# Kernel tuning notes

Measured on AMD Instinct MI355X. Metric: run time of the kernel, lower is better.

The kernel has to match this reference:

```python
import jax, jax.numpy as jnp
import numpy as np

EMBED_DIM = 768
NUM_HEADS = 12
HEAD_DIM = EMBED_DIM // NUM_HEADS
SCALE = HEAD_DIM ** -0.5


def setup_inputs() -> dict:
    key = jax.random.key(0)
    k_x, k_qw, k_qb, k_pw, k_pb = jax.random.split(key, 5)
    B, N, C = 8, 1024, EMBED_DIM
    std = C ** -0.5
    return {
        "x": jax.random.normal(k_x, (B, N, C), dtype=jnp.float32),
        "qkv_w": jax.random.normal(k_qw, (C, 3 * C), dtype=jnp.float32) * std,
        "qkv_b": jax.random.normal(k_qb, (3 * C,), dtype=jnp.float32) * 0.02,
        "proj_w": jax.random.normal(k_pw, (C, C), dtype=jnp.float32) * std,
        "proj_b": jax.random.normal(k_pb, (C,), dtype=jnp.float32) * 0.02,
    }


def reference(x, qkv_w, qkv_b, proj_w, proj_b):
    B, N, C = x.shape
    # QKV projection: [B,N,3C] -> [3,B,H,N,Dh]
    qkv = (x @ qkv_w + qkv_b).reshape(B, N, 3, NUM_HEADS, HEAD_DIM)
    qkv = jnp.transpose(qkv, (2, 0, 3, 1, 4))
    q, k, v = qkv[0], qkv[1], qkv[2]
    # attention scores [B,H,N,N]
    attn = jnp.einsum("bhqd,bhkd->bhqk", q, k) * SCALE
    attn_weights = jax.nn.softmax(attn, axis=-1)
    # dropout=0.0 (eval) -> identity
    out = jnp.einsum("bhqk,bhkd->bhqd", attn_weights, v)
    out = jnp.transpose(out, (0, 2, 1, 3)).reshape(B, N, C)
    out = out @ proj_w + proj_b
    return out, attn_weights
```

## Files before the change

### kernel.cpp

```cpp
#include <hip/hip_runtime.h>
#include <cstdint>
#include <cstddef>

namespace {

constexpr int B = 8, NSEQ = 1024, C = 768, H = 12, D = 64, N3 = 2304;
constexpr float SCALE = 0.125f;
constexpr size_t QKV_ELEMS = (size_t)B * H * NSEQ * D;

using f32x4 = __attribute__((ext_vector_type(4))) float;
using s16x8 = __attribute__((ext_vector_type(8))) short;

__device__ __forceinline__ unsigned short f2bf(float f) {
  union { float f; uint32_t u; } v; v.f = f;
  const uint32_t r = v.u + 0x7FFFu + ((v.u >> 16) & 1u);
  return (unsigned short)(r >> 16);
}
__device__ __forceinline__ float bf2f(unsigned short s) {
  union { uint32_t u; float f; } v; v.u = ((uint32_t)s) << 16;
  return v.f;
}
__device__ __forceinline__ void gload_lds16(const void* g, void* l) {
  __builtin_amdgcn_global_load_lds(
      (const __attribute__((address_space(1))) uint32_t*)g,
      (__attribute__((address_space(3))) uint32_t*)l, 16, 0, 0);
}

__global__ void cvt_x(const float* __restrict__ x, unsigned short* __restrict__ xb, int n4) {
  const int stride = gridDim.x * 256;
  for (int idx = blockIdx.x * 256 + threadIdx.x; idx < n4; idx += stride) {
    const float4 v = ((const float4*)x)[idx];
    ushort4 o;
    o.x = f2bf(v.x); o.y = f2bf(v.y); o.z = f2bf(v.z); o.w = f2bf(v.w);
    ((ushort4*)xb)[idx] = o;
  }
}

__global__ void transp_cvt(const float* __restrict__ w, unsigned short* __restrict__ wt,
                           int K, int N) {
  __shared__ float t[32][33];
  const int n0 = blockIdx.x << 5, k0 = blockIdx.y << 5;
  const int tid = threadIdx.x;
  #pragma unroll
  for (int r = 0; r < 4; ++r) {
    const int e = (r << 8) + tid;
    const int kk = e >> 5, nn = e & 31;
    t[kk][nn] = w[(size_t)(k0 + kk) * N + n0 + nn];
  }
  __syncthreads();
  #pragma unroll
  for (int r = 0; r < 4; ++r) {
    const int e = (r << 8) + tid;
    const int nn = e >> 5, kk = e & 31;
    wt[(size_t)(n0 + nn) * K + k0 + kk] = f2bf(t[kk][nn]);
  }
}

template<int MODE>
__global__ __launch_bounds__(256, 2)
void gemm_bf16(const unsigned short* __restrict__ A,
               const unsigned short* __restrict__ Wt,
               const float* __restrict__ bias,
               unsigned short* __restrict__ qp, unsigned short* __restrict__ kp,
               unsigned short* __restrict__ vt, float* __restrict__ out32,
               int M, int N) {
  constexpr int K = 768;
  __shared__ short As[128 * 64];
  __shared__ short Bs[128 * 64];
  const int tid = threadIdx.x;
  const int wid = tid >> 6, lane = tid & 63;
  const int wm = wid >> 1, wn = wid & 1;
  const int lg = lane >> 4, lr = lane & 15;
  const int m0 = blockIdx.y << 7, n0 = blockIdx.x << 7;

  f32x4 acc[4][4] = {};

  for (int k0 = 0; k0 < K; k0 += 64) {
    __syncthreads();
    #pragma unroll
    for (int r = 0; r < 4; ++r) {
      const int c = (r << 8) + tid;
      const int row = c >> 3, g8 = c & 7;
      const int gp = g8 ^ (row & 7);
      const int ldsoff = (((r << 8) + (wid << 6)) << 3);
      gload_lds16(A + (size_t)(m0 + row) * K + k0 + (gp << 3), (void*)(As + ldsoff));
      gload_lds16(Wt + (size_t)(n0 + row) * K + k0 + (gp << 3), (void*)(Bs + ldsoff));
    }
    __syncthreads();
    #pragma unroll
    for (int kc = 0; kc < 2; ++kc) {
      s16x8 af[4], bf[4];
      #pragma unroll
      for (int i = 0; i < 4; ++i) {
        const int ra = (wm << 6) + (i << 4) + lr;
        const int ca = ((kc << 2) + lg) ^ (ra & 7);
        af[i] = *(const s16x8*)(As + (ra << 6) + (ca << 3));
        const int rb = (wn << 6) + (i << 4) + lr;
        const int cb = ((kc << 2) + lg) ^ (rb & 7);
        bf[i] = *(const s16x8*)(Bs + (rb << 6) + (cb << 3));
      }
      #pragma unroll
      for (int i = 0; i < 4; ++i)
        #pragma unroll
        for (int j = 0; j < 4; ++j)
          acc[i][j] = __builtin_amdgcn_mfma_f32_16x16x32_bf16(af[i], bf[j], acc[i][j], 0, 0, 0);
    }
  }

  #pragma unroll
  for (int i = 0; i < 4; ++i) {
    const int m = m0 + (wm << 6) + (i << 4) + (lg << 2);
    #pragma unroll
    for (int j = 0; j < 4; ++j) {
      const int n = n0 + (wn << 6) + (j << 4) + lr;
      const float bv = bias[n];
      if (MODE == 0) {
        const int which = (n >= 1536) ? 2 : (n >= 768 ? 1 : 0);
        const int hh = (n - which * 768) >> 6;
        const int d = n & 63;
        const int b = m >> 10, ns = m & 1023;
        const size_t bh = (size_t)b * H + hh;
        if (which < 2) {
          unsigned short* dst = (which == 0 ? qp : kp) + (bh * NSEQ + ns) * D + d;
          #pragma unroll
          for (int rg = 0; rg < 4; ++rg)
            dst[(size_t)rg * D] = f2bf(acc[i][j][rg] + bv);
        } else {
          ushort4 pk;
          pk.x = f2bf(acc[i][j][0] + bv);
          pk.y = f2bf(acc[i][j][1] + bv);
          pk.z = f2bf(acc[i][j][2] + bv);
          pk.w = f2bf(acc[i][j][3] + bv);
          *(ushort4*)(vt + (bh * D + d) * NSEQ + ns) = pk;
        }
      } else {
        float* dst = out32 + (size_t)m * N + n;
        #pragma unroll
        for (int rg = 0; rg < 4; ++rg)
          dst[(size_t)rg * N] = acc[i][j][rg] + bv;
      }
    }
  }
}

__global__ __launch_bounds__(256, 3)
void attn_mfma(const unsigned short* __restrict__ qg,
               const unsigned short* __restrict__ kg,
               const unsigned short* __restrict__ vtg,
               float* __restrict__ attnw,
               unsigned short* __restrict__ aout) {
  __shared__ short sc[16][1032];
  __shared__ short kv[64 * 64];
  __shared__ float invs[16];
  const int tid = threadIdx.x;
  const int wid = tid >> 6, lane = tid & 63;
  const int lg = lane >> 4, lr = lane & 15;
  const int bh = blockIdx.y;
  const int q0 = blockIdx.x << 4;
  const size_t kvbase = (size_t)bh * NSEQ * D;

  s16x8 qf[2];
  #pragma unroll
  for (int kc = 0; kc < 2; ++kc)
    qf[kc] = *(const s16x8*)(qg + kvbase + (size_t)(q0 + lr) * D + (kc << 5) + (lg << 3));

  for (int j0 = 0; j0 < NSEQ; j0 += 64) {
    __syncthreads();
    #pragma unroll
    for (int r = 0; r < 2; ++r) {
      const int c = (r << 8) + tid;
      const int row = c >> 3, g8 = c & 7;
      gload_lds16(kg + kvbase + (size_t)(j0 + row) * D + ((g8 ^ (row & 7)) << 3),
                  (void*)(kv + (((r << 8) + (wid << 6)) << 3)));
    }
    __syncthreads();
    f32x4 cacc = {};
    const int krow = (wid << 4) + lr;
    #pragma unroll
    for (int kc = 0; kc < 2; ++kc) {
      const int cg = ((kc << 2) + lg) ^ (krow & 7);
      const s16x8 kf = *(const s16x8*)(kv + (krow << 6) + (cg << 3));
      cacc = __builtin_amdgcn_mfma_f32_16x16x32_bf16(qf[kc], kf, cacc, 0, 0, 0);
    }
    const int jglob = j0 + (wid << 4) + lr;
    #pragma unroll
    for (int rg = 0; rg < 4; ++rg)
      sc[(lg << 2) + rg][jglob] = (short)f2bf(cacc[rg] * SCALE);
  }
  __syncthreads();

  {
    const int row = tid >> 4, ql = tid & 15;
    float mx = -3.0e38f;
    #pragma unroll
    for (int c = 0; c < 8; ++c) {
      const s16x8 v = *(const s16x8*)(&sc[row][(ql << 3) + (c << 7)]);
      #pragma unroll
      for (int e = 0; e < 8; ++e) mx = fmaxf(mx, bf2f((unsigned short)v[e]));
    }
    #pragma unroll
    for (int off = 8; off > 0; off >>= 1) mx = fmaxf(mx, __shfl_xor(mx, off, 16));
    float s = 0.f;
    #pragma unroll
    for (int c = 0; c < 8; ++c) {
      s16x8 v = *(s16x8*)(&sc[row][(ql << 3) + (c << 7)]);
      #pragma unroll
      for (int e = 0; e < 8; ++e) {
        const float ev = __expf(bf2f((unsigned short)v[e]) - mx);
        s += ev;
        v[e] = (short)f2bf(ev);
      }
      *(s16x8*)(&sc[row][(ql << 3) + (c << 7)]) = v;
    }
    #pragma unroll
    for (int off = 8; off > 0; off >>= 1) s += __shfl_xor(s, off, 16);
    if (ql == 0) invs[row] = 1.0f / s;
  }
  __syncthreads();

  {
    float* wbase = attnw + ((size_t)bh * NSEQ + q0) * NSEQ;
    #pragma unroll
    for (int r = 0; r < 16; ++r) {
      const float iv = invs[r];
      const ushort4 e4 = *(const ushort4*)(&sc[r][tid << 2]);
      float4 o;
      o.x = bf2f(e4.x) * iv; o.y = bf2f(e4.y) * iv;
      o.z = bf2f(e4.z) * iv; o.w = bf2f(e4.w) * iv;
      *(float4*)(wbase + (size_t)r * NSEQ + (tid << 2)) = o;
    }
  }

  f32x4 oacc = {};
  for (int j0 = 0; j0 < NSEQ; j0 += 64) {
    __syncthreads();
    #pragma unroll
    for (int r = 0; r < 2; ++r) {
      const int c = (r << 8) + tid;
      const int row = c >> 3, g8 = c & 7;
      gload_lds16(vtg + (size_t)bh * D * NSEQ + (size_t)row * NSEQ + j0 + ((g8 ^ (row & 7)) << 3),
                  (void*)(kv + (((r << 8) + (wid << 6)) << 3)));
    }
    __syncthreads();
    const int drow = (wid << 4) + lr;
    #pragma unroll
    for (int kc = 0; kc < 2; ++kc) {
      const s16x8 pa = *(const s16x8*)(&sc[lr][j0 + (kc << 5) + (lg << 3)]);
      const int cg = ((kc << 2) + lg) ^ (drow & 7);
      const s16x8 vf = *(const s16x8*)(kv + (drow << 6) + (cg << 3));
      oacc = __builtin_amdgcn_mfma_f32_16x16x32_bf16(pa, vf, oacc, 0, 0, 0);
    }
  }
  {
    const int b = bh / H, hh = bh - b * H;
    const int d = (wid << 4) + lr;
    #pragma unroll
    for (int rg = 0; rg < 4; ++rg) {
      const int i = (lg << 2) + rg;
      aout[((size_t)b * NSEQ + q0 + i) * C + hh * D + d] = f2bf(oacc[rg] * invs[i]);
    }
  }
}

}

extern "C" void kernel_launch(void* const* d_in, const int* in_sizes, int n_in,
                              void* d_out, int out_size, void* d_ws, size_t ws_size,
                              hipStream_t stream) {
  const float* x      = (const float*)d_in[0];
  const float* qkv_w  = (const float*)d_in[1];
  const float* qkv_b  = (const float*)d_in[2];
  const float* proj_w = (const float*)d_in[3];
  const float* proj_b = (const float*)d_in[4];

  float* out   = (float*)d_out;
  float* attnw = out + (size_t)B * NSEQ * C;

  unsigned short* xb   = (unsigned short*)d_ws;
  unsigned short* wtq  = xb   + (size_t)8192 * 768;
  unsigned short* wtp  = wtq  + (size_t)2304 * 768;
  unsigned short* qp   = wtp  + (size_t)768 * 768;
  unsigned short* kp   = qp   + QKV_ELEMS;
  unsigned short* vtp  = kp   + QKV_ELEMS;
  unsigned short* wsao = vtp  + QKV_ELEMS;

  cvt_x<<<1024, 256, 0, stream>>>(x, xb, (int)((size_t)8192 * 768 / 4));
  transp_cvt<<<dim3(N3 / 32, C / 32), 256, 0, stream>>>(qkv_w, wtq, C, N3);
  transp_cvt<<<dim3(C / 32, C / 32), 256, 0, stream>>>(proj_w, wtp, C, C);

  gemm_bf16<0><<<dim3(N3 / 128, 8192 / 128), 256, 0, stream>>>(
      xb, wtq, qkv_b, qp, kp, vtp, nullptr, 8192, N3);

  attn_mfma<<<dim3(NSEQ / 16, B * H), 256, 0, stream>>>(qp, kp, vtp, attnw, wsao);

  gemm_bf16<1><<<dim3(C / 128, 8192 / 128), 256, 0, stream>>>(
      wsao, wtp, proj_b, nullptr, nullptr, nullptr, out, 8192, C);
}
```

Baseline: 266.6 us.

## Double attention query tile per block and remap blocks across XCDs

The attention kernel now runs 512 threads and handles 32 query rows per block. Each K/V tile loaded into shared memory therefore serves two 16-row query groups, which halves K/V reloads per query. Block indices in both the attention and GEMM kernels are remapped so that neighbouring logical tiles land on the same XCD, aiming for better L2 reuse of shared operands. The attention-weight store moves after the PV product and is widened to 8 elements per thread. The cost is a larger shared-memory footprint (32 score rows) and lower occupancy per block.

After: 283.8 us. 6.4% more time.

```diff
diff --git a/kernel.cpp b/kernel.cpp
--- a/kernel.cpp
+++ b/kernel.cpp
@@ -26,7 +26,8 @@
       (__attribute__((address_space(3))) uint32_t*)l, 16, 0, 0);
 }
 
-__global__ void cvt_x(const float* __restrict__ x, unsigned short* __restrict__ xb, int n4) {
+__global__ __launch_bounds__(256)
+void cvt_x(const float* __restrict__ x, unsigned short* __restrict__ xb, int n4) {
   const int stride = gridDim.x * 256;
   for (int idx = blockIdx.x * 256 + threadIdx.x; idx < n4; idx += stride) {
     const float4 v = ((const float4*)x)[idx];
@@ -36,8 +37,9 @@
   }
 }
 
-__global__ void transp_cvt(const float* __restrict__ w, unsigned short* __restrict__ wt,
-                           int K, int N) {
+__global__ __launch_bounds__(256)
+void transp_cvt(const float* __restrict__ w, unsigned short* __restrict__ wt,
+                int K, int N) {
   __shared__ float t[32][33];
   const int n0 = blockIdx.x << 5, k0 = blockIdx.y << 5;
   const int tid = threadIdx.x;
@@ -63,7 +65,7 @@
                const float* __restrict__ bias,
                unsigned short* __restrict__ qp, unsigned short* __restrict__ kp,
                unsigned short* __restrict__ vt, float* __restrict__ out32,
-               int M, int N) {
+               int N, int NT) {
   constexpr int K = 768;
   __shared__ short As[128 * 64];
   __shared__ short Bs[128 * 64];
@@ -71,7 +73,11 @@
   const int wid = tid >> 6, lane = tid & 63;
   const int wm = wid >> 1, wn = wid & 1;
   const int lg = lane >> 4, lr = lane & 15;
-  const int m0 = blockIdx.y << 7, n0 = blockIdx.x << 7;
+
+  const int cpx = gridDim.x >> 3;
+  const int logical = (blockIdx.x & 7) * cpx + (blockIdx.x >> 3);
+  const int bx = logical % NT, by = logical / NT;
+  const int m0 = by << 7, n0 = bx << 7;
 
   f32x4 acc[4][4] = {};
 
@@ -143,49 +149,52 @@
   }
 }
 
-__global__ __launch_bounds__(256, 3)
+constexpr int RS = 1032;
+
+__global__ __launch_bounds__(512, 4)
 void attn_mfma(const unsigned short* __restrict__ qg,
                const unsigned short* __restrict__ kg,
                const unsigned short* __restrict__ vtg,
                float* __restrict__ attnw,
                unsigned short* __restrict__ aout) {
-  __shared__ short sc[16][1032];
+  __shared__ short sc[32][RS];
   __shared__ short kv[64 * 64];
-  __shared__ float invs[16];
+  __shared__ float invs[32];
   const int tid = threadIdx.x;
   const int wid = tid >> 6, lane = tid & 63;
   const int lg = lane >> 4, lr = lane & 15;
-  const int bh = blockIdx.y;
-  const int q0 = blockIdx.x << 4;
+  const int wq = wid >> 2, ws = wid & 3;
+
+  const int logical = (blockIdx.x & 7) * 384 + (blockIdx.x >> 3);
+  const int bh = logical >> 5;
+  const int q0 = (logical & 31) << 5;
   const size_t kvbase = (size_t)bh * NSEQ * D;
 
   s16x8 qf[2];
   #pragma unroll
   for (int kc = 0; kc < 2; ++kc)
-    qf[kc] = *(const s16x8*)(qg + kvbase + (size_t)(q0 + lr) * D + (kc << 5) + (lg << 3));
+    qf[kc] = *(const s16x8*)(qg + kvbase + (size_t)(q0 + (wq << 4) + lr) * D + (kc << 5) + (lg << 3));
 
   for (int j0 = 0; j0 < NSEQ; j0 += 64) {
     __syncthreads();
-    #pragma unroll
-    for (int r = 0; r < 2; ++r) {
-      const int c = (r << 8) + tid;
-      const int row = c >> 3, g8 = c & 7;
+    {
+      const int row = tid >> 3, g8 = tid & 7;
       gload_lds16(kg + kvbase + (size_t)(j0 + row) * D + ((g8 ^ (row & 7)) << 3),
-                  (void*)(kv + (((r << 8) + (wid << 6)) << 3)));
+                  (void*)(kv + (wid << 9)));
     }
     __syncthreads();
     f32x4 cacc = {};
-    const int krow = (wid << 4) + lr;
+    const int krow = (ws << 4) + lr;
     #pragma unroll
     for (int kc = 0; kc < 2; ++kc) {
       const int cg = ((kc << 2) + lg) ^ (krow & 7);
       const s16x8 kf = *(const s16x8*)(kv + (krow << 6) + (cg << 3));
       cacc = __builtin_amdgcn_mfma_f32_16x16x32_bf16(qf[kc], kf, cacc, 0, 0, 0);
     }
-    const int jglob = j0 + (wid << 4) + lr;
+    const int jg = j0 + (ws << 4) + lr;
     #pragma unroll
     for (int rg = 0; rg < 4; ++rg)
-      sc[(lg << 2) + rg][jglob] = (short)f2bf(cacc[rg] * SCALE);
+      sc[(wq << 4) + (lg << 2) + rg][jg] = (short)f2bf(cacc[rg] * SCALE);
   }
   __syncthreads();
 
@@ -218,46 +227,50 @@
   }
   __syncthreads();
 
-  {
-    float* wbase = attnw + ((size_t)bh * NSEQ + q0) * NSEQ;
-    #pragma unroll
-    for (int r = 0; r < 16; ++r) {
-      const float iv = invs[r];
-      const ushort4 e4 = *(const ushort4*)(&sc[r][tid << 2]);
-      float4 o;
-      o.x = bf2f(e4.x) * iv; o.y = bf2f(e4.y) * iv;
-      o.z = bf2f(e4.z) * iv; o.w = bf2f(e4.w) * iv;
-      *(float4*)(wbase + (size_t)r * NSEQ + (tid << 2)) = o;
-    }
-  }
-
   f32x4 oacc = {};
   for (int j0 = 0; j0 < NSEQ; j0 += 64) {
     __syncthreads();
-    #pragma unroll
-    for (int r = 0; r < 2; ++r) {
-      const int c = (r << 8) + tid;
-      const int row = c >> 3, g8 = c & 7;
+    {
+      const int row = tid >> 3, g8 = tid & 7;
       gload_lds16(vtg + (size_t)bh * D * NSEQ + (size_t)row * NSEQ + j0 + ((g8 ^ (row & 7)) << 3),
-                  (void*)(kv + (((r << 8) + (wid << 6)) << 3)));
-    }
-    __syncthreads();
-    const int drow = (wid << 4) + lr;
+                  (void*)(kv + (wid << 9)));
+    }
+    __syncthreads();
+    const int drow = (ws << 4) + lr;
     #pragma unroll
     for (int kc = 0; kc < 2; ++kc) {
-      const s16x8 pa = *(const s16x8*)(&sc[lr][j0 + (kc << 5) + (lg << 3)]);
+      const s16x8 pa = *(const s16x8*)(&sc[(wq << 4) + lr][j0 + (kc << 5) + (lg << 3)]);
       const int cg = ((kc << 2) + lg) ^ (drow & 7);
       const s16x8 vf = *(const s16x8*)(kv + (drow << 6) + (cg << 3));
       oacc = __builtin_amdgcn_mfma_f32_16x16x32_bf16(pa, vf, oacc, 0, 0, 0);
     }
   }
+
   {
     const int b = bh / H, hh = bh - b * H;
-    const int d = (wid << 4) + lr;
+    const int d = (ws << 4) + lr;
     #pragma unroll
     for (int rg = 0; rg < 4; ++rg) {
-      const int i = (lg << 2) + rg;
-      aout[((size_t)b * NSEQ + q0 + i) * C + hh * D + d] = f2bf(oacc[rg] * invs[i]);
+      const int qi = (wq << 4) + (lg << 2) + rg;
+      aout[((size_t)b * NSEQ + q0 + qi) * C + hh * D + d] = f2bf(oacc[rg] * invs[qi]);
+    }
+  }
+
+  {
+    float* wbase = attnw + ((size_t)bh * NSEQ + q0) * NSEQ;
+    #pragma unroll
+    for (int r = 0; r < 8; ++r) {
+      const int row = (r << 2) + (tid >> 7);
+      const int colb = (tid & 127) << 3;
+      const float iv = invs[row];
+      const s16x8 e8 = *(const s16x8*)(&sc[row][colb]);
+      float4 o0, o1;
+      o0.x = bf2f((unsigned short)e8[0]) * iv; o0.y = bf2f((unsigned short)e8[1]) * iv;
+      o0.z = bf2f((unsigned short)e8[2]) * iv; o0.w = bf2f((unsigned short)e8[3]) * iv;
+      o1.x = bf2f((unsigned short)e8[4]) * iv; o1.y = bf2f((unsigned short)e8[5]) * iv;
+      o1.z = bf2f((unsigned short)e8[6]) * iv; o1.w = bf2f((unsigned short)e8[7]) * iv;
+      *(float4*)(wbase + (size_t)row * NSEQ + colb) = o0;
+      *(float4*)(wbase + (size_t)row * NSEQ + colb + 4) = o1;
     }
   }
 }
@@ -288,11 +301,11 @@
   transp_cvt<<<dim3(N3 / 32, C / 32), 256, 0, stream>>>(qkv_w, wtq, C, N3);
   transp_cvt<<<dim3(C / 32, C / 32), 256, 0, stream>>>(proj_w, wtp, C, C);
 
-  gemm_bf16<0><<<dim3(N3 / 128, 8192 / 128), 256, 0, stream>>>(
-      xb, wtq, qkv_b, qp, kp, vtp, nullptr, 8192, N3);
-
-  attn_mfma<<<dim3(NSEQ / 16, B * H), 256, 0, stream>>>(qp, kp, vtp, attnw, wsao);
-
-  gemm_bf16<1><<<dim3(C / 128, 8192 / 128), 256, 0, stream>>>(
-      wsao, wtp, proj_b, nullptr, nullptr, nullptr, out, 8192, C);
-}
+  gemm_bf16<0><<<(N3 / 128) * (8192 / 128), 256, 0, stream>>>(
+      xb, wtq, qkv_b, qp, kp, vtp, nullptr, N3, N3 / 128);
+
+  attn_mfma<<<(NSEQ / 32) * (B * H), 512, 0, stream>>>(qp, kp, vtp, attnw, wsao);
+
+  gemm_bf16<1><<<(C / 128) * (8192 / 128), 256, 0, stream>>>(
+      wsao, wtp, proj_b, nullptr, nullptr, nullptr, out, C, C / 128);
+}
```
